# Kernel tuning notes

Hardware: AMD Instinct MI355X
Metric: run time of the kernel (lower is better)

## Reference

```python
import jax, jax.numpy as jnp
import numpy as np
import math

N, E, LAT, MUL, HD = 20000, 160000, 128, 16, 32
H = LAT // HD          # 4 heads
D = 9                  # 0e+1o+2e spherical harmonics dim
SLICES = ((0, 1), (1, 4), (4, 9))
TPD = MUL * len(SLICES)


def _mlp(x, W1, b1, W2, b2):
    return jnp.dot(jax.nn.silu(jnp.dot(x, W1) + b1), W2) + b2


def _eq_linear(x, W):
    # block-diagonal per-l channel mixing: x [E, mul, D], W [n_l, mul, mul]
    return jnp.concatenate([jnp.einsum('ji,eim->ejm', W[l], x[:, :, s:t])
                            for l, (s, t) in enumerate(SLICES)], axis=-1)


def _residual(x, x_new, uc):
    co = jax.lax.rsqrt(uc * uc + 1.0)
    return co * x + (uc * co) * x_new


def _vec_rej(feat, dirs):
    d = dirs[:, None, :]
    return feat - (feat * d).sum(-1, keepdims=True) * d


def _so3_ln(x, eps=1e-8):
    # equivariant RMS layernorm per irrep block
    out = []
    for s, t in SLICES:
        blk = x[:, :, s:t]
        rms = jnp.sqrt((blk * blk).sum(-1).mean(-1) + eps)  # [N]
        out.append(blk / rms[:, None, None])
    return jnp.concatenate(out, axis=-1)


def _ln(x, g, b, eps=1e-5):
    mu = x.mean(-1, keepdims=True)
    var = ((x - mu) ** 2).mean(-1, keepdims=True)
    return (x - mu) * jax.lax.rsqrt(var + eps) * g + b


def _forward(h, X, t_ij, spharms, update_coeff, Wtq, Wtk, Wrs_W, Wrs_b, Wq_W, Wq_b, Wk_W, Wk_b, Wre_W, ln_g, ln_b, Wvu,
             gs_W1, gs_b1, gs_W2, gs_b2, gv_W1, gv_b1, gv_W2, gv_b2, gw_W1, gw_b1, gw_W2, gw_b2,
             gt_W1, gt_b1, gt_W2, gt_b2, gsp_W1, gsp_b1, gsp_W2, gsp_b2, md_W1, md_b1, md_W2, md_b2,
             mt_W1, mt_b1, mt_W2, mt_b2, gm_W1, gm_b1, gm_W2, gm_b2,
             edge_center, edge_neighbor, num_nodes):
    uc = update_coeff
    Xn = X[edge_neighbor]                                     # [E, mul, D]
    Xq = _vec_rej(_eq_linear(X[edge_center], Wtq), spharms)
    Xk = _vec_rej(_eq_linear(Xn, Wtk), -spharms)
    # CG scalar contraction (l x l -> 0e, uuu): normalized per-l dot product
    w = jnp.concatenate([(Xq[:, :, s:t] * Xk[:, :, s:t]).sum(-1) / math.sqrt(t - s)
                         for s, t in SLICES], axis=-1)        # [E, 3*mul]
    dt = _mlp(w, gw_W1, gw_b1, gw_W2, gw_b2) * _mlp(t_ij, gt_W1, gt_b1, gt_W2, gt_b2)
    t_ij = _residual(t_ij, dt, uc)
    h_i = h[edge_center]
    h_j = h[edge_neighbor]
    spatial = (t_ij @ Wrs_W + Wrs_b) * _mlp(h_j, gs_W1, gs_b1, gs_W2, gs_b2)
    En = t_ij.shape[0]
    q = (h_i @ Wq_W + Wq_b).reshape(En, H, HD)
    k = (h_j @ Wk_W + Wk_b).reshape(En, H, HD)
    v = _mlp(h_j, gv_W1, gv_b1, gv_W2, gv_b2)
    ta = jax.nn.silu(t_ij @ Wre_W).reshape(En, H, HD)
    alpha = (q * k * ta).sum(-1) / math.sqrt(HD)              # [E, H]
    amax = jax.ops.segment_max(alpha, edge_center, num_segments=num_nodes)
    ex = jnp.exp(alpha - amax[edge_center])
    den = jax.ops.segment_sum(ex, edge_center, num_segments=num_nodes)
    attn = ex / den[edge_center]                              # scatter_softmax
    sea = (attn[:, :, None] * v.reshape(En, H, HD)).reshape(En, LAT)
    combined = sea + spatial
    gates = _mlp(combined, gsp_W1, gsp_b1, gsp_W2, gsp_b2)
    o_s, o_d, o_t = gates[:, :LAT], gates[:, LAT:2 * LAT], gates[:, 2 * LAT:]
    dh = _ln(jax.ops.segment_sum(o_s, edge_center, num_segments=num_nodes), ln_g, ln_b)
    h = _residual(h, dh, uc)
    gd = _mlp(o_d, md_W1, md_b1, md_W2, md_b2)
    gtt = _mlp(o_t, mt_W1, mt_b1, mt_W2, mt_b2)
    dXij = gd[:, :, None] * spharms[:, None, :] + gtt[:, :, None] * Xn
    dX = _so3_ln(jax.ops.segment_sum(dXij, edge_center, num_segments=num_nodes))
    X = _residual(X, dX, uc)
    # EQFF
    Xp = jnp.einsum('nmi,mj->nji', X, Wvu)
    nrm = jnp.sqrt((Xp * Xp).sum(-1) + 1e-12)
    g = _mlp(jnp.concatenate([h, nrm], axis=-1), gm_W1, gm_b1, gm_W2, gm_b2)
    h = h + g[:, :LAT]
    X = X + g[:, LAT:, None] * Xp
    return h, X, t_ij


def setup_inputs() -> dict:
    key = jax.random.key(0)
    ks = jax.random.split(key, 24)

    def mk_mlp(k, din, dout):
        k1, k2 = jax.random.split(k)
        return (jax.random.normal(k1, (din, LAT)) / math.sqrt(din), jnp.zeros((LAT,)),
                jax.random.normal(k2, (LAT, dout)) / math.sqrt(LAT), jnp.zeros((dout,)))

    inp = {
        'h': jax.random.normal(ks[0], (N, LAT)),
        'X': jax.random.normal(ks[1], (N, MUL, D)),
        't_ij': jax.random.normal(ks[2], (E, LAT)),
        'spharms': jax.random.normal(ks[3], (E, D)),
        'update_coeff': jnp.ones((1,), dtype=jnp.float32),
        'Wtq': jax.random.normal(ks[4], (len(SLICES), MUL, MUL)) / math.sqrt(MUL),
        'Wtk': jax.random.normal(ks[5], (len(SLICES), MUL, MUL)) / math.sqrt(MUL),
        'Wrs_W': jax.random.normal(ks[6], (LAT, LAT)) / math.sqrt(LAT),
        'Wrs_b': jnp.zeros((LAT,)),
        'Wq_W': jax.random.normal(ks[7], (LAT, LAT)) / math.sqrt(LAT),
        'Wq_b': jnp.zeros((LAT,)),
        'Wk_W': jax.random.normal(ks[8], (LAT, LAT)) / math.sqrt(LAT),
        'Wk_b': jnp.zeros((LAT,)),
        'Wre_W': jax.random.normal(ks[9], (LAT, LAT)) / math.sqrt(LAT),
        'ln_g': jnp.ones((LAT,)),
        'ln_b': jnp.zeros((LAT,)),
        'Wvu': jax.random.normal(ks[10], (MUL, MUL)) / math.sqrt(MUL),
    }
    for name, din, dout, k in [('gs', LAT, LAT, ks[11]), ('gv', LAT, LAT, ks[12]), ('gw', TPD, LAT, ks[13]),
                               ('gt', LAT, LAT, ks[14]), ('gsp', LAT, 3 * LAT, ks[15]), ('md', LAT, MUL, ks[16]),
                               ('mt', LAT, MUL, ks[17]), ('gm', LAT + MUL, LAT + MUL, ks[18])]:
        W1, b1, W2, b2 = mk_mlp(k, din, dout)
        inp[name + '_W1'], inp[name + '_b1'], inp[name + '_W2'], inp[name + '_b2'] = W1, b1, W2, b2
    inp['edge_center'] = jax.random.randint(ks[19], (E,), 0, N)
    inp['edge_neighbor'] = jax.random.randint(ks[20], (E,), 0, N)
    inp['num_nodes'] = N
    return inp


def reference(h, X, t_ij, spharms, update_coeff, Wtq, Wtk, Wrs_W, Wrs_b, Wq_W, Wq_b, Wk_W, Wk_b, Wre_W, ln_g, ln_b, Wvu,
              gs_W1, gs_b1, gs_W2, gs_b2, gv_W1, gv_b1, gv_W2, gv_b2, gw_W1, gw_b1, gw_W2, gw_b2,
              gt_W1, gt_b1, gt_W2, gt_b2, gsp_W1, gsp_b1, gsp_W2, gsp_b2, md_W1, md_b1, md_W2, md_b2,
              mt_W1, mt_b1, mt_W2, mt_b2, gm_W1, gm_b1, gm_W2, gm_b2,
              edge_center, edge_neighbor, num_nodes):
    return _forward(h, X, t_ij, spharms, update_coeff, Wtq, Wtk, Wrs_W, Wrs_b, Wq_W, Wq_b, Wk_W, Wk_b, Wre_W, ln_g, ln_b, Wvu,
                    gs_W1, gs_b1, gs_W2, gs_b2, gv_W1, gv_b1, gv_W2, gv_b2, gw_W1, gw_b1, gw_W2, gw_b2,
                    gt_W1, gt_b1, gt_W2, gt_b2, gsp_W1, gsp_b1, gsp_W2, gsp_b2, md_W1, md_b1, md_W2, md_b2,
                    mt_W1, mt_b1, mt_W2, mt_b2, gm_W1, gm_b1, gm_W2, gm_b2,
                    edge_center, edge_neighbor, num_nodes)
```

## Files before the change

### kernel.cpp

```cpp
#include <hip/hip_runtime.h>
#include <math.h>

#define N_NODES 20000
#define E_EDGES 160000
#define LAT 128
#define MUL 16
#define DD 9
#define TPD 48

#define WS_Q      ((size_t)0)
#define WS_K      (WS_Q + (size_t)N_NODES*LAT)
#define WS_V      (WS_K + (size_t)N_NODES*LAT)
#define WS_S      (WS_V + (size_t)N_NODES*LAT)
#define WS_W48    (WS_S + (size_t)N_NODES*LAT)
#define WS_SPATB  (WS_W48 + (size_t)E_EDGES*TPD)
#define WS_ALPHA  (WS_SPATB + (size_t)E_EDGES*LAT/2)
#define WS_ZERO   (WS_ALPHA + (size_t)E_EDGES*4)
#define WS_AMAX   WS_ZERO
#define WS_DEN    (WS_AMAX + (size_t)N_NODES*4)
#define WS_HSUM   (WS_DEN + (size_t)N_NODES*4)
#define WS_NDX    (WS_HSUM + (size_t)N_NODES*LAT)
#define WS_END    (WS_NDX + (size_t)N_NODES*MUL*DD)
#define ZERO_CNT  (WS_END - WS_ZERO)
#define WS_WB     WS_END

#define WOFF_WQ   0
#define WOFF_WK   16384
#define WOFF_GV1  32768
#define WOFF_GV2  49152
#define WOFF_GS1  65536
#define WOFF_GS2  81920
#define WOFF_GW1  98304
#define WOFF_GW2  106496
#define WOFF_GT1  122880
#define WOFF_GT2  139264
#define WOFF_WRS  155648
#define WOFF_WRE  172032
#define WOFF_GSP1 188416
#define WOFF_GSP2 204800
#define WOFF_MD1  253952
#define WOFF_MD2  270336
#define WOFF_MT1  272384
#define WOFF_MT2  288768
#define WB_TOTAL  290816

#define DEVI __device__ __forceinline__

typedef short short8 __attribute__((ext_vector_type(8)));
typedef float f32x4 __attribute__((ext_vector_type(4)));

DEVI float silu_f(float x){ return x / (1.f + __expf(-x)); }
DEVI unsigned int fmap(float x){ unsigned int b=__float_as_uint(x); return (b&0x80000000u)? ~b : (b|0x80000000u); }
DEVI float funmap(unsigned int u){ return (u&0x80000000u)? __uint_as_float(u&0x7fffffffu) : __uint_as_float(~u); }
DEVI unsigned short f2b(float f){ unsigned int u=__float_as_uint(f); return (unsigned short)((u + 0x7fffu + ((u>>16)&1u))>>16); }
DEVI float b2f(unsigned short u){ return __uint_as_float(((unsigned int)u)<<16); }

DEVI void atom_pk(unsigned short* p, unsigned int pk){
  asm volatile("global_atomic_pk_add_bf16 %0, %1, off" :: "v"(p), "v"(pk) : "memory");
}

DEVI f32x4 mfma16(short8 a, short8 b, f32x4 c){
  return __builtin_amdgcn_mfma_f32_16x16x32_bf16(a,b,c,0,0,0);
}

template<int KB>
DEVI void mm_tile2(const unsigned short* act, int strideUS, const unsigned short* Wp,
                   int ntile, int m, int quad, f32x4* acc){
  const unsigned short* wp = Wp + (size_t)ntile*KB*512 + (size_t)quad*128 + m*8;
  const unsigned short* a0 = act + m*strideUS + quad*8;
  const unsigned short* a1 = a0 + 16*strideUS;
  #pragma unroll
  for (int kb=0;kb<KB;++kb){
    short8 bfr = *(const short8*)(wp + (size_t)kb*512);
    short8 af0 = *(const short8*)(a0 + kb*32);
    short8 af1 = *(const short8*)(a1 + kb*32);
    acc[0]=mfma16(af0,bfr,acc[0]);
    acc[1]=mfma16(af1,bfr,acc[1]);
  }
}

template<int KB>
DEVI void mm_tile1(const unsigned short* act, int strideUS, const unsigned short* Wp,
                   int mtbase, int m, int quad, f32x4& acc){
  const unsigned short* wp = Wp + (size_t)quad*128 + m*8;
  const unsigned short* a0 = act + (mtbase*16+m)*strideUS + quad*8;
  #pragma unroll
  for (int kb=0;kb<KB;++kb){
    short8 bfr = *(const short8*)(wp + (size_t)kb*512);
    short8 af  = *(const short8*)(a0 + kb*32);
    acc=mfma16(af,bfr,acc);
  }
}

template<int R, int KD, int LDSTRIDE>
DEVI void mm_acc(const float* src, const float* __restrict__ W, int wstride, int t, float* acc){
  #pragma unroll 2
  for (int k=0;k<KD;k+=4){
    float4 xv[R];
    #pragma unroll
    for (int r=0;r<R;++r) xv[r] = *(const float4*)(src + r*LDSTRIDE + k);
    #pragma unroll
    for (int kk=0;kk<4;++kk){
      float wk = W[(size_t)(k+kk)*wstride + t];
      #pragma unroll
      for (int r=0;r<R;++r) acc[r] += ((const float*)&xv[r])[kk]*wk;
    }
  }
}

__global__ void k0_zero(float* __restrict__ z){
  size_t i = (size_t)blockIdx.x*256 + threadIdx.x;
  if (i < ZERO_CNT) z[i] = 0.f;
}

__global__ __launch_bounds__(256) void k_pack(
  const float* __restrict__ Wq,const float* __restrict__ Wk,
  const float* __restrict__ gv1,const float* __restrict__ gv2,
  const float* __restrict__ gs1,const float* __restrict__ gs2,
  const float* __restrict__ gw1,const float* __restrict__ gw2,
  const float* __restrict__ gt1,const float* __restrict__ gt2,
  const float* __restrict__ Wrs,const float* __restrict__ Wre,
  const float* __restrict__ gsp1,const float* __restrict__ gsp2,
  const float* __restrict__ md1,const float* __restrict__ md2,
  const float* __restrict__ mt1,const float* __restrict__ mt2,
  unsigned short* __restrict__ dst)
{
  int i = blockIdx.x*256 + threadIdx.x;
  if (i >= WB_TOTAL) return;
  const int off[19] = {0,16384,32768,49152,65536,81920,98304,106496,122880,139264,
                       155648,172032,188416,204800,253952,270336,272384,288768,290816};
  int mi=0;
  while (i >= off[mi+1]) ++mi;
  int li = i - off[mi];
  int N = (mi==13)?384:((mi==15||mi==17)?16:128);
  int Ksrc = (mi==6)?48:128;
  int KB = (mi==6)?2:4;
  int j = li&7; int t = li>>3;
  int n_in = t&15; t>>=4;
  int quad = t&3; t>>=2;
  int k_block = t % KB; int n_tile = t / KB;
  int k = k_block*32 + quad*8 + j;
  int n = n_tile*16 + n_in;
  const float* src;
  switch(mi){
    case 0: src=Wq; break;  case 1: src=Wk; break;
    case 2: src=gv1; break; case 3: src=gv2; break;
    case 4: src=gs1; break; case 5: src=gs2; break;
    case 6: src=gw1; break; case 7: src=gw2; break;
    case 8: src=gt1; break; case 9: src=gt2; break;
    case 10: src=Wrs; break; case 11: src=Wre; break;
    case 12: src=gsp1; break; case 13: src=gsp2; break;
    case 14: src=md1; break; case 15: src=md2; break;
    default: src=(mi==16)?mt1:mt2; break;
  }
  float v = (k < Ksrc) ? src[(size_t)k*N + n] : 0.f;
  dst[i] = f2b(v);
}

__global__ __launch_bounds__(256) void k1_node(const float* __restrict__ h,
  const unsigned short* __restrict__ WB,
  const float* __restrict__ Wq_b,const float* __restrict__ Wk_b,
  const float* __restrict__ gv_b1,const float* __restrict__ gv_b2,
  const float* __restrict__ gs_b1,const float* __restrict__ gs_b2,
  float* __restrict__ ws)
{
  __shared__ __align__(16) unsigned short B0[32*136], B1[32*136];
  const int tid=threadIdx.x, lane=tid&63, w=tid>>6, m=lane&15, quad=lane>>4;
  const int n0=blockIdx.x*32;
  for (int idx=tid; idx<4096; idx+=256){ int r=idx>>7,c=idx&127;
    B0[r*136+c]=f2b(h[(size_t)(n0+r)*128+c]); }
  __syncthreads();
  f32x4 z4 = {0.f,0.f,0.f,0.f};
  { f32x4 acc[2][2]={{z4,z4},{z4,z4}};
    #pragma unroll
    for(int i=0;i<2;++i) mm_tile2<4>(B0,136,WB+WOFF_WQ, w*2+i, m, quad, acc[i]);
    #pragma unroll
    for(int i=0;i<2;++i){ int col=(w*2+i)*16+m; float bv=Wq_b[col];
      #pragma unroll
      for(int mt=0;mt<2;++mt)
        #pragma unroll
        for(int r=0;r<4;++r){ int row=mt*16+quad*4+r;
          ws[WS_Q+(size_t)(n0+row)*128+col]=acc[i][mt][r]+bv; } } }
  { f32x4 acc[2][2]={{z4,z4},{z4,z4}};
    #pragma unroll
    for(int i=0;i<2;++i) mm_tile2<4>(B0,136,WB+WOFF_WK, w*2+i, m, quad, acc[i]);
    #pragma unroll
    for(int i=0;i<2;++i){ int col=(w*2+i)*16+m; float bv=Wk_b[col];
      #pragma unroll
      for(int mt=0;mt<2;++mt)
        #pragma unroll
        for(int r=0;r<4;++r){ int row=mt*16+quad*4+r;
          ws[WS_K+(size_t)(n0+row)*128+col]=acc[i][mt][r]+bv; } } }
  { f32x4 acc[2][2]={{z4,z4},{z4,z4}};
    #pragma unroll
    for(int i=0;i<2;++i) mm_tile2<4>(B0,136,WB+WOFF_GV1, w*2+i, m, quad, acc[i]);
    #pragma unroll
    for(int i=0;i<2;++i){ int col=(w*2+i)*16+m; float bv=gv_b1[col];
      #pragma unroll
      for(int mt=0;mt<2;++mt)
        #pragma unroll
        for(int r=0;r<4;++r) B1[(mt*16+quad*4+r)*136+col]=f2b(silu_f(acc[i][mt][r]+bv)); } }
  __syncthreads();
  { f32x4 acc[2][2]={{z4,z4},{z4,z4}};
    #pragma unroll
    for(int i=0;i<2;++i) mm_tile2<4>(B1,136,WB+WOFF_GV2, w*2+i, m, quad, acc[i]);
    #pragma unroll
    for(int i=0;i<2;++i){ int col=(w*2+i)*16+m; float bv=gv_b2[col];
      #pragma unroll
      for(int mt=0;mt<2;++mt)
        #pragma unroll
        for(int r=0;r<4;++r){ int row=mt*16+quad*4+r;
          ws[WS_V+(size_t)(n0+row)*128+col]=acc[i][mt][r]+bv; } } }
  __syncthreads();
  { f32x4 acc[2][2]={{z4,z4},{z4,z4}};
    #pragma unroll
    for(int i=0;i<2;++i) mm_tile2<4>(B0,136,WB+WOFF_GS1, w*2+i, m, quad, acc[i]);
    #pragma unroll
    for(int i=0;i<2;++i){ int col=(w*2+i)*16+m; float bv=gs_b1[col];
      #pragma unroll
      for(int mt=0;mt<2;++mt)
        #pragma unroll
        for(int r=0;r<4;++r) B1[(mt*16+quad*4+r)*136+col]=f2b(silu_f(acc[i][mt][r]+bv)); } }
  __syncthreads();
  { f32x4 acc[2][2]={{z4,z4},{z4,z4}};
    #pragma unroll
    for(int i=0;i<2;++i) mm_tile2<4>(B1,136,WB+WOFF_GS2, w*2+i, m, quad, acc[i]);
    #pragma unroll
    for(int i=0;i<2;++i){ int col=(w*2+i)*16+m; float bv=gs_b2[col];
      #pragma unroll
      for(int mt=0;mt<2;++mt)
        #pragma unroll
        for(int r=0;r<4;++r){ int row=mt*16+quad*4+r;
          ws[WS_S+(size_t)(n0+row)*128+col]=acc[i][mt][r]+bv; } } }
}

__global__ __launch_bounds__(256) void k2_edge_w(
  const float* __restrict__ Xin, const float* __restrict__ sph,
  const float* __restrict__ Wtq, const float* __restrict__ Wtk,
  const int* __restrict__ ec, const int* __restrict__ en, float* __restrict__ ws)
{
  __shared__ float xc[16][144], xn[16][144], sphL[16][9];
  __shared__ float wq[768], wkk[768];
  __shared__ int ceI[16], nbI[16];
  const int tid=threadIdx.x, e0=blockIdx.x*16;
  if (tid<16){ ceI[tid]=ec[e0+tid]; nbI[tid]=en[e0+tid]; }
  for (int idx=tid; idx<768; idx+=256){ wq[idx]=Wtq[idx]; wkk[idx]=Wtk[idx]; }
  __syncthreads();
  for (int idx=tid; idx<2304; idx+=256){ int r=idx/144,c=idx%144;
    xc[r][c]=Xin[(size_t)ceI[r]*144+c]; xn[r][c]=Xin[(size_t)nbI[r]*144+c]; }
  if (tid<144){ int r=tid/9,c=tid%9; sphL[r][c]=sph[(size_t)(e0+r)*9+c]; }
  __syncthreads();
  const int el=tid>>4, j=tid&15;
  float xq[9], xk[9];
  const int ss[3]={0,1,4}, se[3]={1,4,9};
  #pragma unroll
  for (int l=0;l<3;++l){
    for (int mm2=ss[l]; mm2<se[l]; ++mm2){
      float aq=0.f, ak=0.f;
      #pragma unroll
      for (int i=0;i<16;++i){
        float wql = wq[l*256 + j*16 + i], wkl = wkk[l*256 + j*16 + i];
        aq += wql*xc[el][i*9+mm2];
        ak += wkl*xn[el][i*9+mm2];
      }
      xq[mm2]=aq; xk[mm2]=ak;
    }
  }
  float dq=0.f, dk=0.f;
  #pragma unroll
  for (int d=0; d<9; ++d){ dq += xq[d]*sphL[el][d]; dk += xk[d]*sphL[el][d]; }
  #pragma unroll
  for (int d=0; d<9; ++d){ xq[d] -= dq*sphL[el][d]; xk[d] -= dk*sphL[el][d]; }
  const float isc[3] = {1.f, 0.5773502691896258f, 0.4472135954999579f};
  #pragma unroll
  for (int l=0;l<3;++l){
    float s=0.f;
    for (int mm2=ss[l]; mm2<se[l]; ++mm2) s += xq[mm2]*xk[mm2];
    ws[WS_W48 + (size_t)(e0+el)*TPD + l*16 + j] = s*isc[l];
  }
}

__global__ __launch_bounds__(256) void k3_edge_t(
  const float* __restrict__ t_in, const int* __restrict__ ec, const int* __restrict__ en,
  const unsigned short* __restrict__ WB,
  const float* __restrict__ gw_b1,const float* __restrict__ gw_b2,
  const float* __restrict__ gt_b1,const float* __restrict__ gt_b2,
  const float* __restrict__ Wrs_b,
  const float* __restrict__ ucp, float* __restrict__ ws, float* __restrict__ outT)
{
  __shared__ __align__(16) unsigned short tin_b[32*136], hid_b[32*136], tnw_b[32*136], wb_b[32*72];
  __shared__ float qk[32*132];
  __shared__ int ceI[32], nbI[32];
  const int tid=threadIdx.x, lane=tid&63, w=tid>>6, m=lane&15, quad=lane>>4;
  const int e0=blockIdx.x*32;
  if (tid<32){ ceI[tid]=ec[e0+tid]; nbI[tid]=en[e0+tid]; }
  __syncthreads();
  const float* Qp=ws+WS_Q; const float* Kp=ws+WS_K;
  for (int idx=tid; idx<4096; idx+=256){
    int r=idx>>7, c=idx&127;
    tin_b[r*136+c] = f2b(t_in[(size_t)(e0+r)*128+c]);
    qk[r*132+c] = Qp[(size_t)ceI[r]*128+c]*Kp[(size_t)nbI[r]*128+c];
  }
  for (int idx=tid; idx<2048; idx+=256){
    int r=idx>>6, c=idx&63;
    wb_b[r*72+c] = (c<48)? f2b(ws[WS_W48+(size_t)(e0+r)*TPD+c]) : (unsigned short)0;
  }
  __syncthreads();
  const float uc=ucp[0], co=rsqrtf(uc*uc+1.f), ucco=uc*co;
  f32x4 z4 = {0.f,0.f,0.f,0.f};
  { f32x4 acc[2][2]={{z4,z4},{z4,z4}};
    #pragma unroll
    for(int i=0;i<2;++i) mm_tile2<2>(wb_b,72,WB+WOFF_GW1, w*2+i, m, quad, acc[i]);
    #pragma unroll
    for(int i=0;i<2;++i){ int col=(w*2+i)*16+m; float bv=gw_b1[col];
      #pragma unroll
      for(int mt=0;mt<2;++mt)
        #pragma unroll
        for(int r=0;r<4;++r) hid_b[(mt*16+quad*4+r)*136+col]=f2b(silu_f(acc[i][mt][r]+bv)); } }
  __syncthreads();
  f32x4 accw[2][2]={{z4,z4},{z4,z4}};
  #pragma unroll
  for(int i=0;i<2;++i) mm_tile2<4>(hid_b,136,WB+WOFF_GW2, w*2+i, m, quad, accw[i]);
  __syncthreads();
  { f32x4 acc[2][2]={{z4,z4},{z4,z4}};
    #pragma unroll
    for(int i=0;i<2;++i) mm_tile2<4>(tin_b,136,WB+WOFF_GT1, w*2+i, m, quad, acc[i]);
    #pragma unroll
    for(int i=0;i<2;++i){ int col=(w*2+i)*16+m; float bv=gt_b1[col];
      #pragma unroll
      for(int mt=0;mt<2;++mt)
        #pragma unroll
        for(int r=0;r<4;++r) hid_b[(mt*16+quad*4+r)*136+col]=f2b(silu_f(acc[i][mt][r]+bv)); } }
  __syncthreads();
  { f32x4 acct[2][2]={{z4,z4},{z4,z4}};
    #pragma unroll
    for(int i=0;i<2;++i) mm_tile2<4>(hid_b,136,WB+WOFF_GT2, w*2+i, m, quad, acct[i]);
    #pragma unroll
    for(int i=0;i<2;++i){ int col=(w*2+i)*16+m; float bw=gw_b2[col], bt=gt_b2[col];
      #pragma unroll
      for(int mt=0;mt<2;++mt)
        #pragma unroll
        for(int r=0;r<4;++r){ int row=mt*16+quad*4+r;
          float dt=(accw[i][mt][r]+bw)*(acct[i][mt][r]+bt);
          float tn=co*b2f(tin_b[row*136+col]) + ucco*dt;
          tnw_b[row*136+col]=f2b(tn);
          outT[(size_t)(e0+row)*128+col]=tn; } } }
  __syncthreads();
  unsigned short* spatB = (unsigned short*)(ws+WS_SPATB);
  { f32x4 acc[2][2]={{z4,z4},{z4,z4}};
    #pragma unroll
    for(int i=0;i<2;++i) mm_tile2<4>(tnw_b,136,WB+WOFF_WRS, w*2+i, m, quad, acc[i]);
    #pragma unroll
    for(int i=0;i<2;++i){ int col=(w*2+i)*16+m; float bv=Wrs_b[col];
      #pragma unroll
      for(int mt=0;mt<2;++mt)
        #pragma unroll
        for(int r=0;r<4;++r){ int row=mt*16+quad*4+r;
          float sv=ws[WS_S+(size_t)nbI[row]*128+col];
          spatB[(size_t)(e0+row)*128+col]=f2b((acc[i][mt][r]+bv)*sv); } } }
  { f32x4 acc[2][2]={{z4,z4},{z4,z4}};
    #pragma unroll
    for(int i=0;i<2;++i) mm_tile2<4>(tnw_b,136,WB+WOFF_WRE, w*2+i, m, quad, acc[i]);
    unsigned int* amaxu=(unsigned int*)(ws+WS_AMAX);
    #pragma unroll
    for(int mt=0;mt<2;++mt)
      #pragma unroll
      for(int r=0;r<4;++r){ int row=mt*16+quad*4+r;
        float p=0.f;
        #pragma unroll
        for(int i=0;i<2;++i){ int col=(w*2+i)*16+m;
          p += qk[row*132+col]*silu_f(acc[i][mt][r]); }
        p += __shfl_xor(p,1); p += __shfl_xor(p,2); p += __shfl_xor(p,4); p += __shfl_xor(p,8);
        if (m==0){
          float aval = p * 0.17677669529663687f;
          int e=e0+row;
          ws[WS_ALPHA+(size_t)e*4+w]=aval;
          atomicMax(&amaxu[(size_t)ceI[row]*4+w], fmap(aval));
        } } }
}

__global__ __launch_bounds__(256) void k4_softmax(const int* __restrict__ ec, float* __restrict__ ws){
  int i = blockIdx.x*256 + threadIdx.x;
  if (i >= E_EDGES*4) return;
  int e = i>>2, hh = i&3;
  int c = ec[e];
  float a = ws[WS_ALPHA + i];
  const unsigned int* amaxu = (const unsigned int*)(ws + WS_AMAX);
  float am = funmap(amaxu[(size_t)c*4+hh]);
  float exv = __expf(a - am);
  ws[WS_ALPHA + i] = exv;
  atomicAdd(&ws[WS_DEN + (size_t)c*4 + hh], exv);
}

__global__ __launch_bounds__(256) void k5_edge_gate(
  const float* __restrict__ Xin, const float* __restrict__ sph,
  const int* __restrict__ ec, const int* __restrict__ en,
  const unsigned short* __restrict__ WB,
  const float* __restrict__ gsp_b1,const float* __restrict__ gsp_b2,
  const float* __restrict__ md_b1,const float* __restrict__ md_b2,
  const float* __restrict__ mt_b1,const float* __restrict__ mt_b2,
  float* __restrict__ ws)
{
  __shared__ __align__(16) unsigned short B0[32*136], B1[32*136], B2[32*136], B3[32*136];
  __shared__ float gdL[32*16], gtL[32*16], attnL[32*4];
  __shared__ int ceI[32], nbI[32];
  const int tid=threadIdx.x, lane=tid&63, w=tid>>6, m=lane&15, quad=lane>>4;
  const int e0=blockIdx.x*32;
  if (tid<32){ ceI[tid]=ec[e0+tid]; nbI[tid]=en[e0+tid]; }
  __syncthreads();
  if (tid<128){ int r=tid>>2, hh=tid&3;
    attnL[tid] = ws[WS_ALPHA+(size_t)(e0+r)*4+hh] / ws[WS_DEN+(size_t)ceI[r]*4+hh]; }
  __syncthreads();
  const float* Vp=ws+WS_V;
  const unsigned short* spatB=(const unsigned short*)(ws+WS_SPATB);
  for (int idx=tid; idx<4096; idx+=256){ int r=idx>>7,c=idx&127;
    float v = attnL[r*4+(c>>5)]*Vp[(size_t)nbI[r]*128+c] + b2f(spatB[(size_t)(e0+r)*128+c]);
    B0[r*136+c]=f2b(v); }
  __syncthreads();
  f32x4 z4 = {0.f,0.f,0.f,0.f};
  { f32x4 acc[2][2]={{z4,z4},{z4,z4}};
    #pragma unroll
    for(int i=0;i<2;++i) mm_tile2<4>(B0,136,WB+WOFF_GSP1, w*2+i, m, quad, acc[i]);
    #pragma unroll
    for(int i=0;i<2;++i){ int col=(w*2+i)*16+m; float bv=gsp_b1[col];
      #pragma unroll
      for(int mt=0;mt<2;++mt)
        #pragma unroll
        for(int r=0;r<4;++r) B1[(mt*16+quad*4+r)*136+col]=f2b(silu_f(acc[i][mt][r]+bv)); } }
  __syncthreads();
  { f32x4 acc[3][2][2];
    #pragma unroll
    for(int g2=0;g2<3;++g2)
      #pragma unroll
      for(int i=0;i<2;++i){ acc[g2][i][0]=z4; acc[g2][i][1]=z4; }
    #pragma unroll
    for(int g2=0;g2<3;++g2)
      #pragma unroll
      for(int i=0;i<2;++i)
        mm_tile2<4>(B1,136,WB+WOFF_GSP2, g2*8+w*2+i, m, quad, acc[g2][i]);
    unsigned short* hsumB=(unsigned short*)(ws+WS_HSUM);
    #pragma unroll
    for(int i=0;i<2;++i){ int col=(w*2+i)*16+m;
      float bS=gsp_b2[col], bD=gsp_b2[128+col], bT=gsp_b2[256+col];
      #pragma unroll
      for(int mt=0;mt<2;++mt)
        #pragma unroll
        for(int r=0;r<4;++r){ int row=mt*16+quad*4+r;
          float vS = acc[0][i][mt][r]+bS;
          float vO = __shfl_xor(vS,1);
          if(!(m&1)){
            unsigned int pk = ((unsigned int)f2b(vO)<<16) | (unsigned int)f2b(vS);
            atom_pk(hsumB + (size_t)ceI[row]*128 + col, pk);
          }
          B2[row*136+col]=f2b(acc[1][i][mt][r]+bD);
          B3[row*136+col]=f2b(acc[2][i][mt][r]+bT); } } }
  __syncthreads();
  { f32x4 acc[2][2]={{z4,z4},{z4,z4}};
    #pragma unroll
    for(int i=0;i<2;++i) mm_tile2<4>(B2,136,WB+WOFF_MD1, w*2+i, m, quad, acc[i]);
    #pragma unroll
    for(int i=0;i<2;++i){ int col=(w*2+i)*16+m; float bv=md_b1[col];
      #pragma unroll
      for(int mt=0;mt<2;++mt)
        #pragma unroll
        for(int r=0;r<4;++r) B0[(mt*16+quad*4+r)*136+col]=f2b(silu_f(acc[i][mt][r]+bv)); } }
  __syncthreads();
  { f32x4 acc[2][2]={{z4,z4},{z4,z4}};
    #pragma unroll
    for(int i=0;i<2;++i) mm_tile2<4>(B3,136,WB+WOFF_MT1, w*2+i, m, quad, acc[i]);
    #pragma unroll
    for(int i=0;i<2;++i){ int col=(w*2+i)*16+m; float bv=mt_b1[col];
      #pragma unroll
      for(int mt=0;mt<2;++mt)
        #pragma unroll
        for(int r=0;r<4;++r) B2[(mt*16+quad*4+r)*136+col]=f2b(silu_f(acc[i][mt][r]+bv)); } }
  __syncthreads();
  { if (w<2){
      f32x4 a=z4; mm_tile1<4>(B0,136,WB+WOFF_MD2, w, m, quad, a);
      #pragma unroll
      for(int r=0;r<4;++r) gdL[(w*16+quad*4+r)*16+m]=a[r]+md_b2[m];
    } else {
      f32x4 a=z4; mm_tile1<4>(B2,136,WB+WOFF_MT2, w-2, m, quad, a);
      #pragma unroll
      for(int r=0;r<4;++r) gtL[((w-2)*16+quad*4+r)*16+m]=a[r]+mt_b2[m];
    } }
  __syncthreads();
  unsigned short* ndxB=(unsigned short*)(ws+WS_NDX);
  for (int idx=tid; idx<2304; idx+=256){
    int r=idx/72, p=idx-r*72; int c0=2*p, c1=c0+1;
    int mm0=c0/9, d0=c0-mm0*9;
    int mm1=c1/9, d1=c1-mm1*9;
    const float* sphE = sph + (size_t)(e0+r)*9;
    const float* xrow = Xin + (size_t)nbI[r]*144;
    float v0 = gdL[r*16+mm0]*sphE[d0] + gtL[r*16+mm0]*xrow[c0];
    float v1 = gdL[r*16+mm1]*sphE[d1] + gtL[r*16+mm1]*xrow[c1];
    unsigned int pk = ((unsigned int)f2b(v1)<<16) | (unsigned int)f2b(v0);
    atom_pk(ndxB + (size_t)ceI[r]*144 + c0, pk);
  }
}

__global__ __launch_bounds__(128) void k6_node(
  const float* __restrict__ h, const float* __restrict__ Xin,
  const float* __restrict__ ln_g,const float* __restrict__ ln_b,
  const float* __restrict__ Wvu,
  const float* __restrict__ gm_W1,const float* __restrict__ gm_b1,
  const float* __restrict__ gm_W2,const float* __restrict__ gm_b2,
  const float* __restrict__ ucp, const float* __restrict__ ws,
  float* __restrict__ outH, float* __restrict__ outX)
{
  __shared__ float cat[4][144], dxb[4][144], xnw[4][144], xp[4][144], hid[4][LAT];
  __shared__ float red[4][2][2], rinv[4][3], gX[4][16], wvu[256];
  const int t=threadIdx.x, n0=blockIdx.x*4;
  const unsigned short* hsumB=(const unsigned short*)(ws+WS_HSUM);
  const unsigned short* ndxB =(const unsigned short*)(ws+WS_NDX);
  const float uc=ucp[0], co=rsqrtf(uc*uc+1.f), ucco=uc*co;
  for (int idx=t; idx<256; idx+=128) wvu[idx]=Wvu[idx];
  for (int idx=t; idx<576; idx+=128){ int r=idx/144,c=idx%144; dxb[r][c]=b2f(ndxB[(size_t)(n0+r)*144+c]); }
  float xv_[4];
  #pragma unroll
  for (int r=0;r<4;++r){
    float x=b2f(hsumB[(size_t)(n0+r)*LAT+t]); xv_[r]=x;
    float s=x, ss=x*x;
    for (int off=32; off; off>>=1){ s+=__shfl_down(s,off,64); ss+=__shfl_down(ss,off,64); }
    if ((t&63)==0){ red[r][t>>6][0]=s; red[r][t>>6][1]=ss; }
  }
  __syncthreads();
  #pragma unroll
  for (int r=0;r<4;++r){
    float s=red[r][0][0]+red[r][1][0], ss=red[r][0][1]+red[r][1][1];
    float mu=s*(1.f/128.f), var=ss*(1.f/128.f)-mu*mu;
    float dh=(xv_[r]-mu)*rsqrtf(var+1e-5f)*ln_g[t]+ln_b[t];
    cat[r][t]=co*h[(size_t)(n0+r)*LAT+t]+ucco*dh;
  }
  if (t<12){
    int r=t/3, l=t-r*3;
    int s0 = (l==0)?0:((l==1)?1:4);
    int s1 = (l==0)?1:((l==1)?4:9);
    float sum=0.f;
    for (int mm2=0;mm2<16;++mm2)
      for (int d=s0;d<s1;++d){ float v=dxb[r][mm2*9+d]; sum+=v*v; }
    rinv[r][l]=rsqrtf(sum*(1.f/16.f)+1e-8f);
  }
  __syncthreads();
  for (int idx=t; idx<144; idx+=128){
    int d=idx%9; int l=(d==0)?0:((d<4)?1:2);
    #pragma unroll
    for (int r=0;r<4;++r)
      xnw[r][idx]=co*Xin[(size_t)(n0+r)*144+idx]+ucco*dxb[r][idx]*rinv[r][l];
  }
  __syncthreads();
  for (int idx=t; idx<144; idx+=128){
    int j=idx/9, i=idx-j*9;
    #pragma unroll
    for (int r=0;r<4;++r){
      float a=0.f;
      #pragma unroll
      for (int mm2=0;mm2<16;++mm2) a+=xnw[r][mm2*9+i]*wvu[mm2*16+j];
      xp[r][idx]=a;
    }
  }
  __syncthreads();
  if (t<64){ int r=t>>4, j=t&15; float s=1e-12f;
    #pragma unroll
    for (int i=0;i<9;++i){ float v=xp[r][j*9+i]; s+=v*v; }
    cat[r][128+j]=sqrtf(s); }
  __syncthreads();
  { float acc[4]; float b=gm_b1[t];
    #pragma unroll
    for(int r=0;r<4;++r)acc[r]=b;
    mm_acc<4,144,144>(&cat[0][0],gm_W1,LAT,t,acc);
    #pragma unroll
    for(int r=0;r<4;++r) hid[r][t]=silu_f(acc[r]); }
  __syncthreads();
  { float acc[4]; float b=gm_b2[t];
    #pragma unroll
    for(int r=0;r<4;++r)acc[r]=b;
    mm_acc<4,LAT,LAT>(&hid[0][0],gm_W2,144,t,acc);
    #pragma unroll
    for(int r=0;r<4;++r) outH[(size_t)(n0+r)*LAT+t]=cat[r][t]+acc[r]; }
  if (t<16){ float acc[4]; float b=gm_b2[128+t];
    #pragma unroll
    for(int r=0;r<4;++r)acc[r]=b;
    for (int k=0;k<LAT;++k){ float wk=gm_W2[(size_t)k*144+128+t];
      #pragma unroll
      for(int r=0;r<4;++r) acc[r]+=hid[r][k]*wk; }
    #pragma unroll
    for(int r=0;r<4;++r) gX[r][t]=acc[r]; }
  __syncthreads();
  for (int idx=t; idx<144; idx+=128){
    int j=idx/9;
    #pragma unroll
    for (int r=0;r<4;++r)
      outX[(size_t)(n0+r)*144+idx]=xnw[r][idx]+gX[r][j]*xp[r][idx];
  }
}

extern "C" void kernel_launch(void* const* d_in, const int* in_sizes, int n_in,
                              void* d_out, int out_size, void* d_ws, size_t ws_size,
                              hipStream_t stream)
{
  const float* h      = (const float*)d_in[0];
  const float* X      = (const float*)d_in[1];
  const float* t_ij   = (const float*)d_in[2];
  const float* sph    = (const float*)d_in[3];
  const float* ucp    = (const float*)d_in[4];
  const float* Wtq    = (const float*)d_in[5];
  const float* Wtk    = (const float*)d_in[6];
  const float* Wrs_W  = (const float*)d_in[7];
  const float* Wrs_b  = (const float*)d_in[8];
  const float* Wq_W   = (const float*)d_in[9];
  const float* Wq_b   = (const float*)d_in[10];
  const float* Wk_W   = (const float*)d_in[11];
  const float* Wk_b   = (const float*)d_in[12];
  const float* Wre_W  = (const float*)d_in[13];
  const float* ln_g   = (const float*)d_in[14];
  const float* ln_b   = (const float*)d_in[15];
  const float* Wvu    = (const float*)d_in[16];
  const float* gs_W1=(const float*)d_in[17], *gs_b1=(const float*)d_in[18],
             *gs_W2=(const float*)d_in[19], *gs_b2=(const float*)d_in[20];
  const float* gv_W1=(const float*)d_in[21], *gv_b1=(const float*)d_in[22],
             *gv_W2=(const float*)d_in[23], *gv_b2=(const float*)d_in[24];
  const float* gw_W1=(const float*)d_in[25], *gw_b1=(const float*)d_in[26],
             *gw_W2=(const float*)d_in[27], *gw_b2=(const float*)d_in[28];
  const float* gt_W1=(const float*)d_in[29], *gt_b1=(const float*)d_in[30],
             *gt_W2=(const float*)d_in[31], *gt_b2=(const float*)d_in[32];
  const float* gsp_W1=(const float*)d_in[33], *gsp_b1=(const float*)d_in[34],
             *gsp_W2=(const float*)d_in[35], *gsp_b2=(const float*)d_in[36];
  const float* md_W1=(const float*)d_in[37], *md_b1=(const float*)d_in[38],
             *md_W2=(const float*)d_in[39], *md_b2=(const float*)d_in[40];
  const float* mt_W1=(const float*)d_in[41], *mt_b1=(const float*)d_in[42],
             *mt_W2=(const float*)d_in[43], *mt_b2=(const float*)d_in[44];
  const float* gm_W1=(const float*)d_in[45], *gm_b1=(const float*)d_in[46],
             *gm_W2=(const float*)d_in[47], *gm_b2=(const float*)d_in[48];
  const int* ec = (const int*)d_in[49];
  const int* en = (const int*)d_in[50];
  (void)in_sizes; (void)n_in; (void)out_size; (void)ws_size;

  float* ws   = (float*)d_ws;
  unsigned short* WB = (unsigned short*)(ws + WS_WB);
  float* outH = (float*)d_out;
  float* outX = outH + (size_t)N_NODES*LAT;
  float* outT = outX + (size_t)N_NODES*MUL*DD;

  k0_zero<<<dim3((unsigned)((ZERO_CNT+255)/256)), dim3(256), 0, stream>>>(ws + WS_ZERO);
  k_pack<<<dim3((WB_TOTAL+255)/256), dim3(256), 0, stream>>>(
      Wq_W,Wk_W, gv_W1,gv_W2, gs_W1,gs_W2, gw_W1,gw_W2, gt_W1,gt_W2,
      Wrs_W,Wre_W, gsp_W1,gsp_W2, md_W1,md_W2, mt_W1,mt_W2, WB);
  k1_node<<<dim3(N_NODES/32), dim3(256), 0, stream>>>(h, WB, Wq_b, Wk_b,
      gv_b1,gv_b2, gs_b1,gs_b2, ws);
  k2_edge_w<<<dim3(E_EDGES/16), dim3(256), 0, stream>>>(X, sph, Wtq, Wtk, ec, en, ws);
  k3_edge_t<<<dim3(E_EDGES/32), dim3(256), 0, stream>>>(t_ij, ec, en, WB,
      gw_b1,gw_b2, gt_b1,gt_b2, Wrs_b, ucp, ws, outT);
  k4_softmax<<<dim3((E_EDGES*4)/256), dim3(256), 0, stream>>>(ec, ws);
  k5_edge_gate<<<dim3(E_EDGES/32), dim3(256), 0, stream>>>(X, sph, ec, en, WB,
      gsp_b1,gsp_b2, md_b1,md_b2, mt_b1,mt_b2, ws);
  k6_node<<<dim3(N_NODES/4), dim3(128), 0, stream>>>(h, X, ln_g, ln_b, Wvu,
      gm_W1,gm_b1,gm_W2,gm_b2, ucp, ws, outH, outX);
}
```

Measured before the change: 777.6 us.

## Store node Q/K/V/S projections in bf16 and vectorize gathers and conversions

Node-level Q, K, V and S projections are written to the workspace as bf16 instead of fp32. This halves the bytes for the random per-edge gathers of those rows, and the workspace offsets are resized to match. Loads of h, t_in, the w48 features, X rows and the gathered bf16 pairs now use float4/float2/uint vector accesses, with paired bf16 conversion through the HIP intrinsics. The cost is extra rounding of Q, K, V and S before the edge products, which adds some precision loss.

```diff
diff --git a/kernel.cpp b/kernel.cpp
--- a/kernel.cpp
+++ b/kernel.cpp
@@ -1,4 +1,5 @@
 #include <hip/hip_runtime.h>
+#include <hip/hip_bf16.h>
 #include <math.h>
 
 #define N_NODES 20000
@@ -8,19 +9,19 @@
 #define DD 9
 #define TPD 48
 
-#define WS_Q      ((size_t)0)
-#define WS_K      (WS_Q + (size_t)N_NODES*LAT)
-#define WS_V      (WS_K + (size_t)N_NODES*LAT)
-#define WS_S      (WS_V + (size_t)N_NODES*LAT)
-#define WS_W48    (WS_S + (size_t)N_NODES*LAT)
+#define WS_QB     ((size_t)0)
+#define WS_KB     (WS_QB + (size_t)N_NODES*LAT/2)
+#define WS_VB     (WS_KB + (size_t)N_NODES*LAT/2)
+#define WS_SB     (WS_VB + (size_t)N_NODES*LAT/2)
+#define WS_W48    (WS_SB + (size_t)N_NODES*LAT/2)
 #define WS_SPATB  (WS_W48 + (size_t)E_EDGES*TPD)
 #define WS_ALPHA  (WS_SPATB + (size_t)E_EDGES*LAT/2)
 #define WS_ZERO   (WS_ALPHA + (size_t)E_EDGES*4)
 #define WS_AMAX   WS_ZERO
 #define WS_DEN    (WS_AMAX + (size_t)N_NODES*4)
 #define WS_HSUM   (WS_DEN + (size_t)N_NODES*4)
-#define WS_NDX    (WS_HSUM + (size_t)N_NODES*LAT)
-#define WS_END    (WS_NDX + (size_t)N_NODES*MUL*DD)
+#define WS_NDX    (WS_HSUM + (size_t)N_NODES*LAT/2)
+#define WS_END    (WS_NDX + (size_t)N_NODES*72)
 #define ZERO_CNT  (WS_END - WS_ZERO)
 #define WS_WB     WS_END
 
@@ -52,7 +53,15 @@
 DEVI float silu_f(float x){ return x / (1.f + __expf(-x)); }
 DEVI unsigned int fmap(float x){ unsigned int b=__float_as_uint(x); return (b&0x80000000u)? ~b : (b|0x80000000u); }
 DEVI float funmap(unsigned int u){ return (u&0x80000000u)? __uint_as_float(u&0x7fffffffu) : __uint_as_float(~u); }
-DEVI unsigned short f2b(float f){ unsigned int u=__float_as_uint(f); return (unsigned short)((u + 0x7fffu + ((u>>16)&1u))>>16); }
+
+DEVI unsigned short f2b(float f){
+  __hip_bfloat16 hb = __float2bfloat16(f);
+  unsigned short u; __builtin_memcpy(&u,&hb,2); return u;
+}
+DEVI unsigned int f2b2(float lo, float hi){
+  __hip_bfloat162 h2 = __float22bfloat162_rn(make_float2(lo,hi));
+  unsigned int u; __builtin_memcpy(&u,&h2,4); return u;
+}
 DEVI float b2f(unsigned short u){ return __uint_as_float(((unsigned int)u)<<16); }
 
 DEVI void atom_pk(unsigned short* p, unsigned int pk){
@@ -167,9 +176,15 @@
   __shared__ __align__(16) unsigned short B0[32*136], B1[32*136];
   const int tid=threadIdx.x, lane=tid&63, w=tid>>6, m=lane&15, quad=lane>>4;
   const int n0=blockIdx.x*32;
-  for (int idx=tid; idx<4096; idx+=256){ int r=idx>>7,c=idx&127;
-    B0[r*136+c]=f2b(h[(size_t)(n0+r)*128+c]); }
-  __syncthreads();
+  for (int idx=tid; idx<1024; idx+=256){ int r=idx>>5, c4=(idx&31)*4;
+    float4 hv = *(const float4*)(h+(size_t)(n0+r)*128+c4);
+    *(unsigned int*)(B0+r*136+c4)   = f2b2(hv.x,hv.y);
+    *(unsigned int*)(B0+r*136+c4+2) = f2b2(hv.z,hv.w); }
+  __syncthreads();
+  unsigned short* Qb=(unsigned short*)(ws+WS_QB);
+  unsigned short* Kb=(unsigned short*)(ws+WS_KB);
+  unsigned short* Vb=(unsigned short*)(ws+WS_VB);
+  unsigned short* Sb=(unsigned short*)(ws+WS_SB);
   f32x4 z4 = {0.f,0.f,0.f,0.f};
   { f32x4 acc[2][2]={{z4,z4},{z4,z4}};
     #pragma unroll
@@ -180,7 +195,7 @@
       for(int mt=0;mt<2;++mt)
         #pragma unroll
         for(int r=0;r<4;++r){ int row=mt*16+quad*4+r;
-          ws[WS_Q+(size_t)(n0+row)*128+col]=acc[i][mt][r]+bv; } } }
+          Qb[(size_t)(n0+row)*128+col]=f2b(acc[i][mt][r]+bv); } } }
   { f32x4 acc[2][2]={{z4,z4},{z4,z4}};
     #pragma unroll
     for(int i=0;i<2;++i) mm_tile2<4>(B0,136,WB+WOFF_WK, w*2+i, m, quad, acc[i]);
@@ -190,7 +205,7 @@
       for(int mt=0;mt<2;++mt)
         #pragma unroll
         for(int r=0;r<4;++r){ int row=mt*16+quad*4+r;
-          ws[WS_K+(size_t)(n0+row)*128+col]=acc[i][mt][r]+bv; } } }
+          Kb[(size_t)(n0+row)*128+col]=f2b(acc[i][mt][r]+bv); } } }
   { f32x4 acc[2][2]={{z4,z4},{z4,z4}};
     #pragma unroll
     for(int i=0;i<2;++i) mm_tile2<4>(B0,136,WB+WOFF_GV1, w*2+i, m, quad, acc[i]);
@@ -210,7 +225,7 @@
       for(int mt=0;mt<2;++mt)
         #pragma unroll
         for(int r=0;r<4;++r){ int row=mt*16+quad*4+r;
-          ws[WS_V+(size_t)(n0+row)*128+col]=acc[i][mt][r]+bv; } } }
+          Vb[(size_t)(n0+row)*128+col]=f2b(acc[i][mt][r]+bv); } } }
   __syncthreads();
   { f32x4 acc[2][2]={{z4,z4},{z4,z4}};
     #pragma unroll
@@ -231,7 +246,7 @@
       for(int mt=0;mt<2;++mt)
         #pragma unroll
         for(int r=0;r<4;++r){ int row=mt*16+quad*4+r;
-          ws[WS_S+(size_t)(n0+row)*128+col]=acc[i][mt][r]+bv; } } }
+          Sb[(size_t)(n0+row)*128+col]=f2b(acc[i][mt][r]+bv); } } }
 }
 
 __global__ __launch_bounds__(256) void k2_edge_w(
@@ -295,16 +310,22 @@
   const int e0=blockIdx.x*32;
   if (tid<32){ ceI[tid]=ec[e0+tid]; nbI[tid]=en[e0+tid]; }
   __syncthreads();
-  const float* Qp=ws+WS_Q; const float* Kp=ws+WS_K;
-  for (int idx=tid; idx<4096; idx+=256){
-    int r=idx>>7, c=idx&127;
-    tin_b[r*136+c] = f2b(t_in[(size_t)(e0+r)*128+c]);
-    qk[r*132+c] = Qp[(size_t)ceI[r]*128+c]*Kp[(size_t)nbI[r]*128+c];
-  }
-  for (int idx=tid; idx<2048; idx+=256){
-    int r=idx>>6, c=idx&63;
-    wb_b[r*72+c] = (c<48)? f2b(ws[WS_W48+(size_t)(e0+r)*TPD+c]) : (unsigned short)0;
-  }
+  const unsigned short* Qb=(const unsigned short*)(ws+WS_QB);
+  const unsigned short* Kb=(const unsigned short*)(ws+WS_KB);
+  for (int idx=tid; idx<1024; idx+=256){ int r=idx>>5, c4=(idx&31)*4;
+    float4 tv = *(const float4*)(t_in+(size_t)(e0+r)*128+c4);
+    *(unsigned int*)(tin_b+r*136+c4)   = f2b2(tv.x,tv.y);
+    *(unsigned int*)(tin_b+r*136+c4+2) = f2b2(tv.z,tv.w); }
+  for (int idx=tid; idx<2048; idx+=256){ int r=idx>>6, c2=(idx&63)*2;
+    unsigned int qa = *(const unsigned int*)(Qb+(size_t)ceI[r]*128+c2);
+    unsigned int ka = *(const unsigned int*)(Kb+(size_t)nbI[r]*128+c2);
+    float q0=b2f((unsigned short)qa), q1=b2f((unsigned short)(qa>>16));
+    float k0=b2f((unsigned short)ka), k1=b2f((unsigned short)(ka>>16));
+    *(float2*)(qk+r*132+c2) = make_float2(q0*k0, q1*k1); }
+  for (int idx=tid; idx<1152; idx+=256){ int r=idx/36, p=idx-r*36; int c2=p*2;
+    unsigned int v=0u;
+    if (c2<48){ float2 wv=*(const float2*)(ws+WS_W48+(size_t)(e0+r)*TPD+c2); v=f2b2(wv.x,wv.y); }
+    *(unsigned int*)(wb_b+r*72+c2)=v; }
   __syncthreads();
   const float uc=ucp[0], co=rsqrtf(uc*uc+1.f), ucco=uc*co;
   f32x4 z4 = {0.f,0.f,0.f,0.f};
@@ -347,6 +368,7 @@
           outT[(size_t)(e0+row)*128+col]=tn; } } }
   __syncthreads();
   unsigned short* spatB = (unsigned short*)(ws+WS_SPATB);
+  const unsigned short* Sb=(const unsigned short*)(ws+WS_SB);
   { f32x4 acc[2][2]={{z4,z4},{z4,z4}};
     #pragma unroll
     for(int i=0;i<2;++i) mm_tile2<4>(tnw_b,136,WB+WOFF_WRS, w*2+i, m, quad, acc[i]);
@@ -356,7 +378,7 @@
       for(int mt=0;mt<2;++mt)
         #pragma unroll
         for(int r=0;r<4;++r){ int row=mt*16+quad*4+r;
-          float sv=ws[WS_S+(size_t)nbI[row]*128+col];
+          float sv=b2f(Sb[(size_t)nbI[row]*128+col]);
           spatB[(size_t)(e0+row)*128+col]=f2b((acc[i][mt][r]+bv)*sv); } } }
   { f32x4 acc[2][2]={{z4,z4},{z4,z4}};
     #pragma unroll
@@ -411,11 +433,15 @@
   if (tid<128){ int r=tid>>2, hh=tid&3;
     attnL[tid] = ws[WS_ALPHA+(size_t)(e0+r)*4+hh] / ws[WS_DEN+(size_t)ceI[r]*4+hh]; }
   __syncthreads();
-  const float* Vp=ws+WS_V;
+  const unsigned short* Vb=(const unsigned short*)(ws+WS_VB);
   const unsigned short* spatB=(const unsigned short*)(ws+WS_SPATB);
-  for (int idx=tid; idx<4096; idx+=256){ int r=idx>>7,c=idx&127;
-    float v = attnL[r*4+(c>>5)]*Vp[(size_t)nbI[r]*128+c] + b2f(spatB[(size_t)(e0+r)*128+c]);
-    B0[r*136+c]=f2b(v); }
+  for (int idx=tid; idx<2048; idx+=256){ int r=idx>>6, c2=(idx&63)*2;
+    unsigned int va = *(const unsigned int*)(Vb+(size_t)nbI[r]*128+c2);
+    unsigned int sp = *(const unsigned int*)(spatB+(size_t)(e0+r)*128+c2);
+    float a = attnL[r*4+(c2>>5)];
+    float v0 = a*b2f((unsigned short)va) + b2f((unsigned short)sp);
+    float v1 = a*b2f((unsigned short)(va>>16)) + b2f((unsigned short)(sp>>16));
+    *(unsigned int*)(B0+r*136+c2) = f2b2(v0,v1); }
   __syncthreads();
   f32x4 z4 = {0.f,0.f,0.f,0.f};
   { f32x4 acc[2][2]={{z4,z4},{z4,z4}};
@@ -449,8 +475,7 @@
           float vS = acc[0][i][mt][r]+bS;
           float vO = __shfl_xor(vS,1);
           if(!(m&1)){
-            unsigned int pk = ((unsigned int)f2b(vO)<<16) | (unsigned int)f2b(vS);
-            atom_pk(hsumB + (size_t)ceI[row]*128 + col, pk);
+            atom_pk(hsumB + (size_t)ceI[row]*128 + col, f2b2(vS,vO));
           }
           B2[row*136+col]=f2b(acc[1][i][mt][r]+bD);
           B3[row*136+col]=f2b(acc[2][i][mt][r]+bT); } } }
@@ -492,10 +517,10 @@
     int mm1=c1/9, d1=c1-mm1*9;
     const float* sphE = sph + (size_t)(e0+r)*9;
     const float* xrow = Xin + (size_t)nbI[r]*144;
-    float v0 = gdL[r*16+mm0]*sphE[d0] + gtL[r*16+mm0]*xrow[c0];
-    float v1 = gdL[r*16+mm1]*sphE[d1] + gtL[r*16+mm1]*xrow[c1];
-    unsigned int pk = ((unsigned int)f2b(v1)<<16) | (unsigned int)f2b(v0);
-    atom_pk(ndxB + (size_t)ceI[r]*144 + c0, pk);
+    float2 xv = *(const float2*)(xrow+c0);
+    float v0 = gdL[r*16+mm0]*sphE[d0] + gtL[r*16+mm0]*xv.x;
+    float v1 = gdL[r*16+mm1]*sphE[d1] + gtL[r*16+mm1]*xv.y;
+    atom_pk(ndxB + (size_t)ceI[r]*144 + c0, f2b2(v0,v1));
   }
 }
 
```

Measured after the change: 837.7 us. 1.08x slower.
